# Optimization experiments

Hardware: AMD Instinct MI355X
Metric: run time of the kernel (lower is better)

Reference implementation:

```python
import jax, jax.numpy as jnp
import numpy as np

NUM_USERS = 100000
NUM_ITEMS = 100000
EMB_DIM = 128
NUM_LAYERS = 3
NUM_EDGES = 600000
N_NODES = NUM_USERS + NUM_ITEMS


def setup_inputs() -> dict:
    key = jax.random.key(0)
    k_e, k_w = jax.random.split(key)
    edge_index = jax.random.randint(k_e, (2, NUM_EDGES), 0, N_NODES, dtype=jnp.int64)
    # xavier_uniform for Embedding weight [N, D]
    limit = float(np.sqrt(6.0 / (N_NODES + EMB_DIM)))
    emb_weight = jax.random.uniform(k_w, (N_NODES, EMB_DIM), dtype=jnp.float32,
                                    minval=-limit, maxval=limit)
    return {"edge_index": edge_index, "emb_weight": emb_weight}


def _lightgcn_conv(x, row, col):
    # deg[i] = number of edges with col == i (in-degree under source_to_target flow)
    deg = jax.ops.segment_sum(jnp.ones(row.shape[0], dtype=x.dtype), col,
                              num_segments=N_NODES)
    deg_inv_sqrt = jnp.where(deg > 0, jax.lax.rsqrt(jnp.maximum(deg, 1)), 0.0).astype(x.dtype)
    norm = deg_inv_sqrt[row] * deg_inv_sqrt[col]            # [E]
    msg = norm[:, None] * x[row]                             # [E, D] gather + scale
    return jax.ops.segment_sum(msg, col, num_segments=N_NODES)  # scatter-add


def reference(edge_index, emb_weight):
    row, col = edge_index[0], edge_index[1]
    x = emb_weight
    acc = x
    for _ in range(NUM_LAYERS):
        x = _lightgcn_conv(x, row, col)
        acc = acc + x
    embeddings = acc / (NUM_LAYERS + 1)  # mean over stacked layer outputs
    return embeddings[:NUM_USERS], embeddings[NUM_USERS:]
```

## Files before the change

### kernel.cpp

```cpp
#include <hip/hip_runtime.h>

#define NUM_USERS 100000
#define NUM_ITEMS 100000
#define EMB_DIM   128
#define NUM_EDGES 600000
#define NN        200000

#define SCAN_B  256
#define SCAN_NB ((NN + SCAN_B - 1) / SCAN_B)

typedef __attribute__((ext_vector_type(8))) unsigned short ushort8_t;
typedef __attribute__((ext_vector_type(4))) float float4_t;

__device__ inline float bf2f(unsigned short u) {
    unsigned int x = ((unsigned int)u) << 16;
    return __builtin_bit_cast(float, x);
}
__device__ inline unsigned short f2bf(float f) {
    unsigned int x = __builtin_bit_cast(unsigned int, f);
    x += 0x7fffu + ((x >> 16) & 1u);
    return (unsigned short)(x >> 16);
}

__global__ void k_conv(const float* __restrict__ emb, ushort* __restrict__ x0) {
    int i = blockIdx.x * blockDim.x + threadIdx.x;
    const float4 v = reinterpret_cast<const float4*>(emb)[i];
    ushort4 w;
    w.x = f2bf(v.x); w.y = f2bf(v.y); w.z = f2bf(v.z); w.w = f2bf(v.w);
    reinterpret_cast<ushort4*>(x0)[i] = w;
}

__global__ void k_count(const int* __restrict__ col, int* __restrict__ deg) {
    int e = blockIdx.x * blockDim.x + threadIdx.x;
    if (e < NUM_EDGES) atomicAdd(&deg[col[e]], 1);
}

__global__ void k_scan1(const int* __restrict__ deg, int* __restrict__ rp,
                        int* __restrict__ bsum, float* __restrict__ dis) {
    __shared__ int s[SCAN_B];
    int tid = threadIdx.x;
    int i = blockIdx.x * SCAN_B + tid;
    int v = (i < NN) ? deg[i] : 0;
    s[tid] = v;
    __syncthreads();
    for (int off = 1; off < SCAN_B; off <<= 1) {
        int t = (tid >= off) ? s[tid - off] : 0;
        __syncthreads();
        s[tid] += t;
        __syncthreads();
    }
    if (i < NN) {
        rp[i]  = s[tid] - v;
        dis[i] = (v > 0) ? 1.0f / sqrtf((float)v) : 0.0f;
    }
    if (tid == SCAN_B - 1) bsum[blockIdx.x] = s[tid];
}

__global__ void k_scan2(int* __restrict__ bsum) {
    __shared__ int s[1024];
    int tid = threadIdx.x;
    int v = (tid < SCAN_NB) ? bsum[tid] : 0;
    s[tid] = v;
    __syncthreads();
    for (int off = 1; off < 1024; off <<= 1) {
        int t = (tid >= off) ? s[tid - off] : 0;
        __syncthreads();
        s[tid] += t;
        __syncthreads();
    }
    if (tid < SCAN_NB) bsum[tid] = s[tid] - v;
}

__global__ void k_scan3(int* __restrict__ rp, const int* __restrict__ bsum) {
    int i = blockIdx.x * SCAN_B + threadIdx.x;
    if (i < NN) rp[i] += bsum[blockIdx.x];
    if (i == 0) rp[NN] = NUM_EDGES;
}

__global__ void k_fill(const int* __restrict__ row, const int* __restrict__ col,
                       const float* __restrict__ dis, const int* __restrict__ rp,
                       int* __restrict__ cursor, int2* __restrict__ csr) {
    int e = blockIdx.x * blockDim.x + threadIdx.x;
    if (e >= NUM_EDGES) return;
    int r = row[e], c = col[e];
    int p = rp[c] + atomicAdd(&cursor[c], 1);
    csr[p] = make_int2(r, __builtin_bit_cast(int, dis[r] * dis[c]));
}

__global__ void k_gath(const ushort* __restrict__ x, const int* __restrict__ rp,
                       const int2* __restrict__ csr, ushort* __restrict__ xn) {
    int t    = blockIdx.x * blockDim.x + threadIdx.x;
    int node = t >> 4;
    int lane = t & 15;
    if (node >= NN) return;
    int beg = rp[node], end = rp[node + 1];
    float a[8] = {0, 0, 0, 0, 0, 0, 0, 0};
    const int bd = lane * 8;
    for (int k = beg; k < end; k += 4) {
        const int last = end - 1;
        const int k1 = min(k + 1, last), k2 = min(k + 2, last), k3 = min(k + 3, last);
        const int2 e0 = csr[k], e1 = csr[k1], e2 = csr[k2], e3 = csr[k3];
        const float c0 = __builtin_bit_cast(float, e0.y);
        const float c1 = (k + 1 <= last) ? __builtin_bit_cast(float, e1.y) : 0.0f;
        const float c2 = (k + 2 <= last) ? __builtin_bit_cast(float, e2.y) : 0.0f;
        const float c3 = (k + 3 <= last) ? __builtin_bit_cast(float, e3.y) : 0.0f;
        const ushort8_t v0 = *reinterpret_cast<const ushort8_t*>(x + (size_t)e0.x * EMB_DIM + bd);
        const ushort8_t v1 = *reinterpret_cast<const ushort8_t*>(x + (size_t)e1.x * EMB_DIM + bd);
        const ushort8_t v2 = *reinterpret_cast<const ushort8_t*>(x + (size_t)e2.x * EMB_DIM + bd);
        const ushort8_t v3 = *reinterpret_cast<const ushort8_t*>(x + (size_t)e3.x * EMB_DIM + bd);
#pragma unroll
        for (int j = 0; j < 8; ++j)
            a[j] += c0 * bf2f(v0[j]) + c1 * bf2f(v1[j]) +
                    c2 * bf2f(v2[j]) + c3 * bf2f(v3[j]);
    }
    ushort8_t w;
#pragma unroll
    for (int j = 0; j < 8; ++j) w[j] = f2bf(a[j]);
    *reinterpret_cast<ushort8_t*>(xn + (size_t)node * EMB_DIM + bd) = w;
}

__global__ void k_final(const ushort* __restrict__ x2, const int* __restrict__ rp,
                        const int2* __restrict__ csr,
                        const ushort* __restrict__ x0, const ushort* __restrict__ x1,
                        float* __restrict__ out) {
    int t    = blockIdx.x * blockDim.x + threadIdx.x;
    int node = t >> 4;
    int lane = t & 15;
    if (node >= NN) return;
    int beg = rp[node], end = rp[node + 1];
    float a[8] = {0, 0, 0, 0, 0, 0, 0, 0};
    const int bd = lane * 8;
    for (int k = beg; k < end; k += 4) {
        const int last = end - 1;
        const int k1 = min(k + 1, last), k2 = min(k + 2, last), k3 = min(k + 3, last);
        const int2 e0 = csr[k], e1 = csr[k1], e2 = csr[k2], e3 = csr[k3];
        const float c0 = __builtin_bit_cast(float, e0.y);
        const float c1 = (k + 1 <= last) ? __builtin_bit_cast(float, e1.y) : 0.0f;
        const float c2 = (k + 2 <= last) ? __builtin_bit_cast(float, e2.y) : 0.0f;
        const float c3 = (k + 3 <= last) ? __builtin_bit_cast(float, e3.y) : 0.0f;
        const ushort8_t v0 = *reinterpret_cast<const ushort8_t*>(x2 + (size_t)e0.x * EMB_DIM + bd);
        const ushort8_t v1 = *reinterpret_cast<const ushort8_t*>(x2 + (size_t)e1.x * EMB_DIM + bd);
        const ushort8_t v2 = *reinterpret_cast<const ushort8_t*>(x2 + (size_t)e2.x * EMB_DIM + bd);
        const ushort8_t v3 = *reinterpret_cast<const ushort8_t*>(x2 + (size_t)e3.x * EMB_DIM + bd);
#pragma unroll
        for (int j = 0; j < 8; ++j)
            a[j] += c0 * bf2f(v0[j]) + c1 * bf2f(v1[j]) +
                    c2 * bf2f(v2[j]) + c3 * bf2f(v3[j]);
    }
    const size_t o = (size_t)node * EMB_DIM + bd;
    const ushort8_t w0 = *reinterpret_cast<const ushort8_t*>(x0 + o);
    const ushort8_t w1 = *reinterpret_cast<const ushort8_t*>(x1 + o);
    const ushort8_t w2 = *reinterpret_cast<const ushort8_t*>(x2 + o);
    float4_t r0, r1;
#pragma unroll
    for (int j = 0; j < 4; ++j)
        r0[j] = (bf2f(w0[j]) + bf2f(w1[j]) + bf2f(w2[j]) + a[j]) * 0.25f;
#pragma unroll
    for (int j = 0; j < 4; ++j)
        r1[j] = (bf2f(w0[j + 4]) + bf2f(w1[j + 4]) + bf2f(w2[j + 4]) + a[j + 4]) * 0.25f;
    __builtin_nontemporal_store(r0, reinterpret_cast<float4_t*>(out + o));
    __builtin_nontemporal_store(r1, reinterpret_cast<float4_t*>(out + o) + 1);
}

extern "C" void kernel_launch(void* const* d_in, const int* in_sizes, int n_in,
                              void* d_out, int out_size, void* d_ws, size_t ws_size,
                              hipStream_t stream) {
    const int*   edges = (const int*)d_in[0];
    const int*   row   = edges;
    const int*   col   = edges + NUM_EDGES;
    const float* emb   = (const float*)d_in[1];
    float*       out   = (float*)d_out;

    char*  ws  = (char*)d_ws;
    size_t off = 0;
    auto alloc = [&](size_t bytes) {
        void* p = ws + off;
        off += (bytes + 255) & ~(size_t)255;
        return p;
    };
    ushort* x0     = (ushort*)alloc(sizeof(ushort) * (size_t)NN * EMB_DIM);
    ushort* x1     = (ushort*)alloc(sizeof(ushort) * (size_t)NN * EMB_DIM);
    ushort* x2     = (ushort*)alloc(sizeof(ushort) * (size_t)NN * EMB_DIM);
    int*    deg    = (int*)   alloc(sizeof(int)   * NN);
    float*  dis    = (float*) alloc(sizeof(float) * NN);
    int*    rp     = (int*)   alloc(sizeof(int)   * (NN + 1));
    int*    cursor = (int*)   alloc(sizeof(int)   * NN);
    int2*   csr    = (int2*)  alloc(sizeof(int2)  * NUM_EDGES);
    int*    bsum   = (int*)   alloc(sizeof(int)   * 1024);

    (void)hipMemsetAsync(deg,    0, sizeof(int) * NN, stream);
    (void)hipMemsetAsync(cursor, 0, sizeof(int) * NN, stream);

    const int EB = (NUM_EDGES + 255) / 256;
    const int CB = (int)(((size_t)NN * EMB_DIM / 4) / 256);
    k_conv<<<CB, 256, 0, stream>>>(emb, x0);
    k_count<<<EB, 256, 0, stream>>>(col, deg);
    k_scan1<<<SCAN_NB, SCAN_B, 0, stream>>>(deg, rp, bsum, dis);
    k_scan2<<<1, 1024, 0, stream>>>(bsum);
    k_scan3<<<SCAN_NB, SCAN_B, 0, stream>>>(rp, bsum);
    k_fill<<<EB, 256, 0, stream>>>(row, col, dis, rp, cursor, csr);

    const int LB = (int)(((size_t)NN * 16) / 256);
    k_gath <<<LB, 256, 0, stream>>>(x0, rp, csr, x1);
    k_gath <<<LB, 256, 0, stream>>>(x1, rp, csr, x2);
    k_final<<<LB, 256, 0, stream>>>(x2, rp, csr, x0, x1, out);
}
```

Measured before the change: 220.6 us.

## Drop bf16 conversion pass; gather fp32 embeddings directly in first layer

Removes the separate fp32-to-bf16 conversion kernel and its x0 buffer. The first propagation layer now gathers fp32 rows straight from the embedding table, and the final kernel reads the fp32 embedding for the layer-0 term. It also merges the two memsets into one by placing deg and cursor next to each other, and switches intermediate writes to nontemporal stores. The cost is that the first-layer gather moves twice as many bytes per edge, while one full streaming pass over the table is saved.

```diff
diff --git a/kernel.cpp b/kernel.cpp
--- a/kernel.cpp
+++ b/kernel.cpp
@@ -20,14 +20,6 @@
     unsigned int x = __builtin_bit_cast(unsigned int, f);
     x += 0x7fffu + ((x >> 16) & 1u);
     return (unsigned short)(x >> 16);
-}
-
-__global__ void k_conv(const float* __restrict__ emb, ushort* __restrict__ x0) {
-    int i = blockIdx.x * blockDim.x + threadIdx.x;
-    const float4 v = reinterpret_cast<const float4*>(emb)[i];
-    ushort4 w;
-    w.x = f2bf(v.x); w.y = f2bf(v.y); w.z = f2bf(v.z); w.w = f2bf(v.w);
-    reinterpret_cast<ushort4*>(x0)[i] = w;
 }
 
 __global__ void k_count(const int* __restrict__ col, int* __restrict__ deg) {
@@ -85,6 +77,47 @@
     int r = row[e], c = col[e];
     int p = rp[c] + atomicAdd(&cursor[c], 1);
     csr[p] = make_int2(r, __builtin_bit_cast(int, dis[r] * dis[c]));
+}
+
+__global__ void k_gath0(const float* __restrict__ emb, const int* __restrict__ rp,
+                        const int2* __restrict__ csr, ushort* __restrict__ xn) {
+    int t    = blockIdx.x * blockDim.x + threadIdx.x;
+    int node = t >> 4;
+    int lane = t & 15;
+    if (node >= NN) return;
+    int beg = rp[node], end = rp[node + 1];
+    float a[8] = {0, 0, 0, 0, 0, 0, 0, 0};
+    const int bd = lane * 8;
+    for (int k = beg; k < end; k += 4) {
+        const int last = end - 1;
+        const int k1 = min(k + 1, last), k2 = min(k + 2, last), k3 = min(k + 3, last);
+        const int2 e0 = csr[k], e1 = csr[k1], e2 = csr[k2], e3 = csr[k3];
+        const float c0 = __builtin_bit_cast(float, e0.y);
+        const float c1 = (k + 1 <= last) ? __builtin_bit_cast(float, e1.y) : 0.0f;
+        const float c2 = (k + 2 <= last) ? __builtin_bit_cast(float, e2.y) : 0.0f;
+        const float c3 = (k + 3 <= last) ? __builtin_bit_cast(float, e3.y) : 0.0f;
+        const float4 u0 = *reinterpret_cast<const float4*>(emb + (size_t)e0.x * EMB_DIM + bd);
+        const float4 u1 = *reinterpret_cast<const float4*>(emb + (size_t)e1.x * EMB_DIM + bd);
+        const float4 u2 = *reinterpret_cast<const float4*>(emb + (size_t)e2.x * EMB_DIM + bd);
+        const float4 u3 = *reinterpret_cast<const float4*>(emb + (size_t)e3.x * EMB_DIM + bd);
+        const float4 w0 = *reinterpret_cast<const float4*>(emb + (size_t)e0.x * EMB_DIM + bd + 4);
+        const float4 w1 = *reinterpret_cast<const float4*>(emb + (size_t)e1.x * EMB_DIM + bd + 4);
+        const float4 w2 = *reinterpret_cast<const float4*>(emb + (size_t)e2.x * EMB_DIM + bd + 4);
+        const float4 w3 = *reinterpret_cast<const float4*>(emb + (size_t)e3.x * EMB_DIM + bd + 4);
+        a[0] += c0 * u0.x + c1 * u1.x + c2 * u2.x + c3 * u3.x;
+        a[1] += c0 * u0.y + c1 * u1.y + c2 * u2.y + c3 * u3.y;
+        a[2] += c0 * u0.z + c1 * u1.z + c2 * u2.z + c3 * u3.z;
+        a[3] += c0 * u0.w + c1 * u1.w + c2 * u2.w + c3 * u3.w;
+        a[4] += c0 * w0.x + c1 * w1.x + c2 * w2.x + c3 * w3.x;
+        a[5] += c0 * w0.y + c1 * w1.y + c2 * w2.y + c3 * w3.y;
+        a[6] += c0 * w0.z + c1 * w1.z + c2 * w2.z + c3 * w3.z;
+        a[7] += c0 * w0.w + c1 * w1.w + c2 * w2.w + c3 * w3.w;
+    }
+    ushort8_t w;
+#pragma unroll
+    for (int j = 0; j < 8; ++j) w[j] = f2bf(a[j]);
+    __builtin_nontemporal_store(w,
+        reinterpret_cast<ushort8_t*>(xn + (size_t)node * EMB_DIM + bd));
 }
 
 __global__ void k_gath(const ushort* __restrict__ x, const int* __restrict__ rp,
@@ -116,12 +149,13 @@
     ushort8_t w;
 #pragma unroll
     for (int j = 0; j < 8; ++j) w[j] = f2bf(a[j]);
-    *reinterpret_cast<ushort8_t*>(xn + (size_t)node * EMB_DIM + bd) = w;
+    __builtin_nontemporal_store(w,
+        reinterpret_cast<ushort8_t*>(xn + (size_t)node * EMB_DIM + bd));
 }
 
 __global__ void k_final(const ushort* __restrict__ x2, const int* __restrict__ rp,
                         const int2* __restrict__ csr,
-                        const ushort* __restrict__ x0, const ushort* __restrict__ x1,
+                        const float* __restrict__ emb, const ushort* __restrict__ x1,
                         float* __restrict__ out) {
     int t    = blockIdx.x * blockDim.x + threadIdx.x;
     int node = t >> 4;
@@ -148,16 +182,19 @@
                     c2 * bf2f(v2[j]) + c3 * bf2f(v3[j]);
     }
     const size_t o = (size_t)node * EMB_DIM + bd;
-    const ushort8_t w0 = *reinterpret_cast<const ushort8_t*>(x0 + o);
+    const float4    e0 = *reinterpret_cast<const float4*>(emb + o);
+    const float4    e1 = *reinterpret_cast<const float4*>(emb + o + 4);
     const ushort8_t w1 = *reinterpret_cast<const ushort8_t*>(x1 + o);
     const ushort8_t w2 = *reinterpret_cast<const ushort8_t*>(x2 + o);
     float4_t r0, r1;
-#pragma unroll
-    for (int j = 0; j < 4; ++j)
-        r0[j] = (bf2f(w0[j]) + bf2f(w1[j]) + bf2f(w2[j]) + a[j]) * 0.25f;
-#pragma unroll
-    for (int j = 0; j < 4; ++j)
-        r1[j] = (bf2f(w0[j + 4]) + bf2f(w1[j + 4]) + bf2f(w2[j + 4]) + a[j + 4]) * 0.25f;
+    r0[0] = (e0.x + bf2f(w1[0]) + bf2f(w2[0]) + a[0]) * 0.25f;
+    r0[1] = (e0.y + bf2f(w1[1]) + bf2f(w2[1]) + a[1]) * 0.25f;
+    r0[2] = (e0.z + bf2f(w1[2]) + bf2f(w2[2]) + a[2]) * 0.25f;
+    r0[3] = (e0.w + bf2f(w1[3]) + bf2f(w2[3]) + a[3]) * 0.25f;
+    r1[0] = (e1.x + bf2f(w1[4]) + bf2f(w2[4]) + a[4]) * 0.25f;
+    r1[1] = (e1.y + bf2f(w1[5]) + bf2f(w2[5]) + a[5]) * 0.25f;
+    r1[2] = (e1.z + bf2f(w1[6]) + bf2f(w2[6]) + a[6]) * 0.25f;
+    r1[3] = (e1.w + bf2f(w1[7]) + bf2f(w2[7]) + a[7]) * 0.25f;
     __builtin_nontemporal_store(r0, reinterpret_cast<float4_t*>(out + o));
     __builtin_nontemporal_store(r1, reinterpret_cast<float4_t*>(out + o) + 1);
 }
@@ -178,22 +215,18 @@
         off += (bytes + 255) & ~(size_t)255;
         return p;
     };
-    ushort* x0     = (ushort*)alloc(sizeof(ushort) * (size_t)NN * EMB_DIM);
     ushort* x1     = (ushort*)alloc(sizeof(ushort) * (size_t)NN * EMB_DIM);
     ushort* x2     = (ushort*)alloc(sizeof(ushort) * (size_t)NN * EMB_DIM);
     int*    deg    = (int*)   alloc(sizeof(int)   * NN);
+    int*    cursor = (int*)   alloc(sizeof(int)   * NN);
     float*  dis    = (float*) alloc(sizeof(float) * NN);
     int*    rp     = (int*)   alloc(sizeof(int)   * (NN + 1));
-    int*    cursor = (int*)   alloc(sizeof(int)   * NN);
     int2*   csr    = (int2*)  alloc(sizeof(int2)  * NUM_EDGES);
     int*    bsum   = (int*)   alloc(sizeof(int)   * 1024);
 
-    (void)hipMemsetAsync(deg,    0, sizeof(int) * NN, stream);
-    (void)hipMemsetAsync(cursor, 0, sizeof(int) * NN, stream);
+    (void)hipMemsetAsync(deg, 0, sizeof(int) * NN * 2, stream);
 
     const int EB = (NUM_EDGES + 255) / 256;
-    const int CB = (int)(((size_t)NN * EMB_DIM / 4) / 256);
-    k_conv<<<CB, 256, 0, stream>>>(emb, x0);
     k_count<<<EB, 256, 0, stream>>>(col, deg);
     k_scan1<<<SCAN_NB, SCAN_B, 0, stream>>>(deg, rp, bsum, dis);
     k_scan2<<<1, 1024, 0, stream>>>(bsum);
@@ -201,7 +234,7 @@
     k_fill<<<EB, 256, 0, stream>>>(row, col, dis, rp, cursor, csr);
 
     const int LB = (int)(((size_t)NN * 16) / 256);
-    k_gath <<<LB, 256, 0, stream>>>(x0, rp, csr, x1);
+    k_gath0<<<LB, 256, 0, stream>>>(emb, rp, csr, x1);
     k_gath <<<LB, 256, 0, stream>>>(x1, rp, csr, x2);
-    k_final<<<LB, 256, 0, stream>>>(x2, rp, csr, x0, x1, out);
-}
+    k_final<<<LB, 256, 0, stream>>>(x2, rp, csr, emb, x1, out);
+}
```

New measurement: 223.6 us. No clear change (+1.4%).

## Fuse conversion and degree count, merge memsets, widen gather to 16 dims per thread

Applied to the files above, without the earlier changes.

Merges the bf16 conversion kernel and the degree-count kernel into one launch that picks its role by block index. The deg and cursor buffers are now adjacent, so a single memset clears both. The gather kernel now uses 8 threads per node, each handling 16 dims with two 16-byte loads per neighbour, which halves the redundant CSR index loads per node but also halves thread-level parallelism and raises register use.

```diff
diff --git a/kernel.cpp b/kernel.cpp
--- a/kernel.cpp
+++ b/kernel.cpp
@@ -9,6 +9,9 @@
 #define SCAN_B  256
 #define SCAN_NB ((NN + SCAN_B - 1) / SCAN_B)
 
+#define CONV_NB 25000
+#define CNT_NB  ((NUM_EDGES + 255) / 256)
+
 typedef __attribute__((ext_vector_type(8))) unsigned short ushort8_t;
 typedef __attribute__((ext_vector_type(4))) float float4_t;
 
@@ -22,17 +25,19 @@
     return (unsigned short)(x >> 16);
 }
 
-__global__ void k_conv(const float* __restrict__ emb, ushort* __restrict__ x0) {
-    int i = blockIdx.x * blockDim.x + threadIdx.x;
-    const float4 v = reinterpret_cast<const float4*>(emb)[i];
-    ushort4 w;
-    w.x = f2bf(v.x); w.y = f2bf(v.y); w.z = f2bf(v.z); w.w = f2bf(v.w);
-    reinterpret_cast<ushort4*>(x0)[i] = w;
-}
-
-__global__ void k_count(const int* __restrict__ col, int* __restrict__ deg) {
-    int e = blockIdx.x * blockDim.x + threadIdx.x;
-    if (e < NUM_EDGES) atomicAdd(&deg[col[e]], 1);
+__global__ void k_setup(const float* __restrict__ emb, ushort* __restrict__ x0,
+                        const int* __restrict__ col, int* __restrict__ deg) {
+    int b = blockIdx.x;
+    if (b < CONV_NB) {
+        int i = b * 256 + threadIdx.x;
+        const float4 v = reinterpret_cast<const float4*>(emb)[i];
+        ushort4 w;
+        w.x = f2bf(v.x); w.y = f2bf(v.y); w.z = f2bf(v.z); w.w = f2bf(v.w);
+        reinterpret_cast<ushort4*>(x0)[i] = w;
+    } else {
+        int e = (b - CONV_NB) * 256 + threadIdx.x;
+        if (e < NUM_EDGES) atomicAdd(&deg[col[e]], 1);
+    }
 }
 
 __global__ void k_scan1(const int* __restrict__ deg, int* __restrict__ rp,
@@ -90,12 +95,12 @@
 __global__ void k_gath(const ushort* __restrict__ x, const int* __restrict__ rp,
                        const int2* __restrict__ csr, ushort* __restrict__ xn) {
     int t    = blockIdx.x * blockDim.x + threadIdx.x;
-    int node = t >> 4;
-    int lane = t & 15;
+    int node = t >> 3;
+    int lane = t & 7;
     if (node >= NN) return;
     int beg = rp[node], end = rp[node + 1];
-    float a[8] = {0, 0, 0, 0, 0, 0, 0, 0};
-    const int bd = lane * 8;
+    float a[16] = {0};
+    const int bd = lane * 16;
     for (int k = beg; k < end; k += 4) {
         const int last = end - 1;
         const int k1 = min(k + 1, last), k2 = min(k + 2, last), k3 = min(k + 3, last);
@@ -104,19 +109,32 @@
         const float c1 = (k + 1 <= last) ? __builtin_bit_cast(float, e1.y) : 0.0f;
         const float c2 = (k + 2 <= last) ? __builtin_bit_cast(float, e2.y) : 0.0f;
         const float c3 = (k + 3 <= last) ? __builtin_bit_cast(float, e3.y) : 0.0f;
-        const ushort8_t v0 = *reinterpret_cast<const ushort8_t*>(x + (size_t)e0.x * EMB_DIM + bd);
-        const ushort8_t v1 = *reinterpret_cast<const ushort8_t*>(x + (size_t)e1.x * EMB_DIM + bd);
-        const ushort8_t v2 = *reinterpret_cast<const ushort8_t*>(x + (size_t)e2.x * EMB_DIM + bd);
-        const ushort8_t v3 = *reinterpret_cast<const ushort8_t*>(x + (size_t)e3.x * EMB_DIM + bd);
-#pragma unroll
-        for (int j = 0; j < 8; ++j)
-            a[j] += c0 * bf2f(v0[j]) + c1 * bf2f(v1[j]) +
-                    c2 * bf2f(v2[j]) + c3 * bf2f(v3[j]);
-    }
-    ushort8_t w;
-#pragma unroll
-    for (int j = 0; j < 8; ++j) w[j] = f2bf(a[j]);
-    *reinterpret_cast<ushort8_t*>(xn + (size_t)node * EMB_DIM + bd) = w;
+        const ushort* p0 = x + (size_t)e0.x * EMB_DIM + bd;
+        const ushort* p1 = x + (size_t)e1.x * EMB_DIM + bd;
+        const ushort* p2 = x + (size_t)e2.x * EMB_DIM + bd;
+        const ushort* p3 = x + (size_t)e3.x * EMB_DIM + bd;
+        const ushort8_t v0a = *reinterpret_cast<const ushort8_t*>(p0);
+        const ushort8_t v1a = *reinterpret_cast<const ushort8_t*>(p1);
+        const ushort8_t v2a = *reinterpret_cast<const ushort8_t*>(p2);
+        const ushort8_t v3a = *reinterpret_cast<const ushort8_t*>(p3);
+        const ushort8_t v0b = *reinterpret_cast<const ushort8_t*>(p0 + 8);
+        const ushort8_t v1b = *reinterpret_cast<const ushort8_t*>(p1 + 8);
+        const ushort8_t v2b = *reinterpret_cast<const ushort8_t*>(p2 + 8);
+        const ushort8_t v3b = *reinterpret_cast<const ushort8_t*>(p3 + 8);
+#pragma unroll
+        for (int j = 0; j < 8; ++j) {
+            a[j]     += c0 * bf2f(v0a[j]) + c1 * bf2f(v1a[j]) +
+                        c2 * bf2f(v2a[j]) + c3 * bf2f(v3a[j]);
+            a[j + 8] += c0 * bf2f(v0b[j]) + c1 * bf2f(v1b[j]) +
+                        c2 * bf2f(v2b[j]) + c3 * bf2f(v3b[j]);
+        }
+    }
+    ushort8_t wa, wb;
+#pragma unroll
+    for (int j = 0; j < 8; ++j) { wa[j] = f2bf(a[j]); wb[j] = f2bf(a[j + 8]); }
+    ushort* q = xn + (size_t)node * EMB_DIM + bd;
+    *reinterpret_cast<ushort8_t*>(q)     = wa;
+    *reinterpret_cast<ushort8_t*>(q + 8) = wb;
 }
 
 __global__ void k_final(const ushort* __restrict__ x2, const int* __restrict__ rp,
@@ -182,26 +200,23 @@
     ushort* x1     = (ushort*)alloc(sizeof(ushort) * (size_t)NN * EMB_DIM);
     ushort* x2     = (ushort*)alloc(sizeof(ushort) * (size_t)NN * EMB_DIM);
     int*    deg    = (int*)   alloc(sizeof(int)   * NN);
+    int*    cursor = (int*)   alloc(sizeof(int)   * NN);
     float*  dis    = (float*) alloc(sizeof(float) * NN);
     int*    rp     = (int*)   alloc(sizeof(int)   * (NN + 1));
-    int*    cursor = (int*)   alloc(sizeof(int)   * NN);
     int2*   csr    = (int2*)  alloc(sizeof(int2)  * NUM_EDGES);
     int*    bsum   = (int*)   alloc(sizeof(int)   * 1024);
 
-    (void)hipMemsetAsync(deg,    0, sizeof(int) * NN, stream);
-    (void)hipMemsetAsync(cursor, 0, sizeof(int) * NN, stream);
-
-    const int EB = (NUM_EDGES + 255) / 256;
-    const int CB = (int)(((size_t)NN * EMB_DIM / 4) / 256);
-    k_conv<<<CB, 256, 0, stream>>>(emb, x0);
-    k_count<<<EB, 256, 0, stream>>>(col, deg);
+    (void)hipMemsetAsync(deg, 0, sizeof(int) * NN * 2, stream);
+
+    k_setup<<<CONV_NB + CNT_NB, 256, 0, stream>>>(emb, x0, col, deg);
     k_scan1<<<SCAN_NB, SCAN_B, 0, stream>>>(deg, rp, bsum, dis);
     k_scan2<<<1, 1024, 0, stream>>>(bsum);
     k_scan3<<<SCAN_NB, SCAN_B, 0, stream>>>(rp, bsum);
-    k_fill<<<EB, 256, 0, stream>>>(row, col, dis, rp, cursor, csr);
-
-    const int LB = (int)(((size_t)NN * 16) / 256);
-    k_gath <<<LB, 256, 0, stream>>>(x0, rp, csr, x1);
-    k_gath <<<LB, 256, 0, stream>>>(x1, rp, csr, x2);
-    k_final<<<LB, 256, 0, stream>>>(x2, rp, csr, x0, x1, out);
-}
+    k_fill<<<CNT_NB, 256, 0, stream>>>(row, col, dis, rp, cursor, csr);
+
+    const int GB = (int)(((size_t)NN * 8)  / 256);
+    const int FB = (int)(((size_t)NN * 16) / 256);
+    k_gath <<<GB, 256, 0, stream>>>(x0, rp, csr, x1);
+    k_gath <<<GB, 256, 0, stream>>>(x1, rp, csr, x2);
+    k_final<<<FB, 256, 0, stream>>>(x2, rp, csr, x0, x1, out);
+}
```

Measured after the change: 221.7 us. Within noise of the previous version (+0.5%).
